# Kernel tuning notes

Hardware: AMD Instinct MI355X
Metric: run time of the kernel (lower is better)

The kernel has to match this reference:

```python
import jax, jax.numpy as jnp
import numpy as np

C = 256
G = 16
KS = 3
K = KS * KS
Cg = C // G
OFFSET_SCALE = 1.0
MLP_HIDDEN = int(C * 4.0)
EPS = 1e-5


def layer_norm(x, w, b):
    mu = jnp.mean(x, axis=-1, keepdims=True)
    xc = x - mu
    var = jnp.mean(xc * xc, axis=-1, keepdims=True)
    return xc * jax.lax.rsqrt(var + EPS) * w + b


def setup_inputs() -> dict:
    key = jax.random.key(0)
    ks = jax.random.split(key, 16)
    B, H, W = 4, 64, 64
    s = 0.02
    inp = {
        "x": jax.random.normal(ks[0], (B, C, H, W), dtype=jnp.float32),
        "norm1_w": jnp.ones((C,), jnp.float32),
        "norm1_b": jnp.zeros((C,), jnp.float32),
        "vproj_w": s * jax.random.normal(ks[1], (C, C), jnp.float32),
        "vproj_b": jnp.zeros((C,), jnp.float32),
        "om_w": s * jax.random.normal(ks[2], (G * 3 * K, C), jnp.float32),
        "om_b": jnp.zeros((G * 3 * K,), jnp.float32),
        "oproj_w": s * jax.random.normal(ks[3], (C, C), jnp.float32),
        "oproj_b": jnp.zeros((C,), jnp.float32),
        "norm2_w": jnp.ones((C,), jnp.float32),
        "norm2_b": jnp.zeros((C,), jnp.float32),
        "fc1_w": s * jax.random.normal(ks[4], (MLP_HIDDEN, C), jnp.float32),
        "fc1_b": jnp.zeros((MLP_HIDDEN,), jnp.float32),
        "fc2_w": s * jax.random.normal(ks[5], (C, MLP_HIDDEN), jnp.float32),
        "fc2_b": jnp.zeros((C,), jnp.float32),
    }
    return inp


def dcnv4(xn, H, W, vproj_w, vproj_b, om_w, om_b, oproj_w, oproj_b):
    # xn: (B, L, C) layer-normed input, L = H*W row-major (h, w)
    B, L, _ = xn.shape
    v = (xn @ vproj_w.T + vproj_b).reshape(B, L, G, Cg)          # value, grouped
    om = (xn @ om_w.T + om_b).reshape(B, L, G, 3 * K)
    off = om[..., : 2 * K].reshape(B, L, G, K, 2)                # (x, y) offsets
    mask = om[..., 2 * K :]                                      # (B, L, G, K) - DCNv4: no softmax

    # kernel grid (dilation 1, 3x3 centered)
    d = jnp.arange(KS, dtype=jnp.float32) - (KS - 1) / 2.0
    dy, dx = jnp.meshgrid(d, d, indexing="ij")                  # (KS, KS)
    dx = dx.reshape(K)
    dy = dy.reshape(K)

    base_x = jnp.tile(jnp.arange(W, dtype=jnp.float32), H)       # (L,)
    base_y = jnp.repeat(jnp.arange(H, dtype=jnp.float32), W)     # (L,)

    # absolute sampling coords in pixel units, (B, L, G, K)
    px = base_x[None, :, None, None] + OFFSET_SCALE * (dx[None, None, None, :] + off[..., 0])
    py = base_y[None, :, None, None] + OFFSET_SCALE * (dy[None, None, None, :] + off[..., 1])

    x0 = jnp.floor(px)
    y0 = jnp.floor(py)
    tx = px - x0
    ty = py - y0
    x0i = x0.astype(jnp.int32)
    y0i = y0.astype(jnp.int32)

    bi = jnp.arange(B)[:, None, None, None]
    gi = jnp.arange(G)[None, None, :, None]

    def gather(xi, yi):
        valid = (xi >= 0) & (xi < W) & (yi >= 0) & (yi < H)
        lin = jnp.clip(yi, 0, H - 1) * W + jnp.clip(xi, 0, W - 1)
        g = v[bi, lin, gi]                                       # (B, L, G, K, Cg)
        return g * valid[..., None].astype(v.dtype)

    samp = (
        gather(x0i, y0i) * ((1 - tx) * (1 - ty))[..., None]
        + gather(x0i + 1, y0i) * (tx * (1 - ty))[..., None]
        + gather(x0i, y0i + 1) * ((1 - tx) * ty)[..., None]
        + gather(x0i + 1, y0i + 1) * (tx * ty)[..., None]
    )
    out = jnp.einsum("blgkc,blgk->blgc", samp, mask).reshape(B, L, C)
    return out @ oproj_w.T + oproj_b


def reference(x, norm1_w, norm1_b, vproj_w, vproj_b, om_w, om_b, oproj_w, oproj_b,
              norm2_w, norm2_b, fc1_w, fc1_b, fc2_w, fc2_b):
    B, _, H, W = x.shape
    shortcut = x.transpose(0, 2, 3, 1).reshape(B, H * W, C)
    xn = layer_norm(shortcut, norm1_w, norm1_b)
    x1 = shortcut + dcnv4(xn, H, W, vproj_w, vproj_b, om_w, om_b, oproj_w, oproj_b)
    h = layer_norm(x1, norm2_w, norm2_b)
    h = jax.nn.gelu(h @ fc1_w.T + fc1_b, approximate=False) @ fc2_w.T + fc2_b
    x2 = x1 + h
    return x2.reshape(B, H, W, C).transpose(0, 3, 1, 2)
```

## Files before the change

### kernel.cpp

```cpp
#include <hip/hip_runtime.h>
#include <math.h>

#define Cc    256
#define Gg    16
#define KK    9
#define Cgc   16
#define Hh    64
#define Ww    64
#define Ll    4096
#define Bb    4
#define HID   1024
#define OMN   432
#define NTOK  16384

typedef unsigned short ushort_t;
typedef __attribute__((ext_vector_type(8))) short bf16x8;
typedef __attribute__((ext_vector_type(4))) float f32x4;

__device__ __forceinline__ ushort_t f2bf(float x) {
    unsigned int u = __float_as_uint(x);
    unsigned int r = (u + 0x7fffu + ((u >> 16) & 1u)) >> 16;
    return (ushort_t)r;
}
__device__ __forceinline__ float bf2f(ushort_t h) {
    return __uint_as_float(((unsigned int)h) << 16);
}
__device__ __forceinline__ void split2(float x, ushort_t& h, ushort_t& l) {
    h = f2bf(x);
    l = f2bf(x - bf2f(h));
}

__global__ void transpose_k(const float* __restrict__ in, float* __restrict__ out,
                            int Rows, int Cols) {
    __shared__ float tile[32][33];
    int b  = blockIdx.z;
    int c0 = blockIdx.x * 32;
    int r0 = blockIdx.y * 32;
    int tx = threadIdx.x;
    int ty = threadIdx.y;
    const float* ip = in + ((size_t)b * Rows + r0) * Cols + c0;
#pragma unroll
    for (int i = 0; i < 32; i += 8)
        tile[ty + i][tx] = ip[(size_t)(ty + i) * Cols + tx];
    __syncthreads();
    float* op = out + ((size_t)b * Cols + c0) * Rows + r0;
#pragma unroll
    for (int i = 0; i < 32; i += 8)
        op[(size_t)(ty + i) * Rows + tx] = tile[tx][ty + i];
}

__global__ void layernorm_k(const float* __restrict__ in, const float* __restrict__ w,
                            const float* __restrict__ bvec,
                            ushort_t* __restrict__ outh, ushort_t* __restrict__ outl) {
    int row  = blockIdx.x * 4 + (threadIdx.x >> 6);
    int lane = threadIdx.x & 63;
    const float4* ip = (const float4*)(in + (size_t)row * Cc);
    float4 v = ip[lane];
    float s  = v.x + v.y + v.z + v.w;
    float sq = v.x * v.x + v.y * v.y + v.z * v.z + v.w * v.w;
#pragma unroll
    for (int m = 1; m < 64; m <<= 1) {
        s  += __shfl_xor(s, m);
        sq += __shfl_xor(sq, m);
    }
    float mu  = s * (1.0f / Cc);
    float var = sq * (1.0f / Cc) - mu * mu;
    float rs  = rsqrtf(var + 1e-5f);
    float4 wv = ((const float4*)w)[lane];
    float4 bv = ((const float4*)bvec)[lane];
    float o0 = (v.x - mu) * rs * wv.x + bv.x;
    float o1 = (v.y - mu) * rs * wv.y + bv.y;
    float o2 = (v.z - mu) * rs * wv.z + bv.z;
    float o3 = (v.w - mu) * rs * wv.w + bv.w;
    ushort4 hv, lv;
    split2(o0, hv.x, lv.x);
    split2(o1, hv.y, lv.y);
    split2(o2, hv.z, lv.z);
    split2(o3, hv.w, lv.w);
    ((ushort4*)(outh + (size_t)row * Cc))[lane] = hv;
    ((ushort4*)(outl + (size_t)row * Cc))[lane] = lv;
}

__global__ void wsplit_k(const float* __restrict__ in,
                         ushort_t* __restrict__ h, ushort_t* __restrict__ l) {
    int i = blockIdx.x * 256 + threadIdx.x;
    float4 v = ((const float4*)in)[i];
    ushort4 hv, lv;
    split2(v.x, hv.x, lv.x);
    split2(v.y, hv.y, lv.y);
    split2(v.z, hv.z, lv.z);
    split2(v.w, hv.w, lv.w);
    ((ushort4*)h)[i] = hv;
    ((ushort4*)l)[i] = lv;
}

template<bool RES, int ACT, int OUT>
__global__ __launch_bounds__(512)
void gemm_mfma_k(const ushort_t* __restrict__ Ah, const ushort_t* __restrict__ Al,
                 const ushort_t* __restrict__ Wh, const ushort_t* __restrict__ Wl,
                 const float* __restrict__ bias, const float* __restrict__ res,
                 float* __restrict__ Cout, ushort_t* __restrict__ Ch,
                 ushort_t* __restrict__ Cl, int M, int N, int Kd) {
    __shared__ ushort_t AsH[128][40];
    __shared__ ushort_t AsL[128][40];
    __shared__ ushort_t BsH[128][40];
    __shared__ ushort_t BsL[128][40];

    int tid  = threadIdx.x;
    int lane = tid & 63;
    int wave = tid >> 6;
    int wm = wave >> 1;
    int wn = wave & 1;
    int m0 = blockIdx.x * 128;
    int n0 = blockIdx.y * 128;

    f32x4 acc[2][4];
#pragma unroll
    for (int i = 0; i < 2; ++i)
#pragma unroll
        for (int j = 0; j < 4; ++j)
#pragma unroll
            for (int r = 0; r < 4; ++r) acc[i][j][r] = 0.0f;

    int lr = tid >> 2;
    int lc = tid & 3;

    int fr = lane & 15;
    int ko = (lane >> 4) * 8;

    for (int k0 = 0; k0 < Kd; k0 += 32) {
        {
            const ushort_t* p = Ah + (size_t)(m0 + lr) * Kd + k0 + lc * 8;
            const ushort_t* q = Al + (size_t)(m0 + lr) * Kd + k0 + lc * 8;
            *(bf16x8*)&AsH[lr][lc * 8] = *(const bf16x8*)p;
            *(bf16x8*)&AsL[lr][lc * 8] = *(const bf16x8*)q;
        }
        {
            bf16x8 z;
#pragma unroll
            for (int t = 0; t < 8; ++t) z[t] = 0;
            int n1 = n0 + lr;
            bf16x8 bh = z, bl = z;
            if (n1 < N) {
                bh = *(const bf16x8*)(Wh + (size_t)n1 * Kd + k0 + lc * 8);
                bl = *(const bf16x8*)(Wl + (size_t)n1 * Kd + k0 + lc * 8);
            }
            *(bf16x8*)&BsH[lr][lc * 8] = bh;
            *(bf16x8*)&BsL[lr][lc * 8] = bl;
        }
        __syncthreads();

        bf16x8 ah[2], al[2], bh[4], bl[4];
#pragma unroll
        for (int i = 0; i < 2; ++i) {
            ah[i] = *(const bf16x8*)&AsH[wm * 32 + i * 16 + fr][ko];
            al[i] = *(const bf16x8*)&AsL[wm * 32 + i * 16 + fr][ko];
        }
#pragma unroll
        for (int j = 0; j < 4; ++j) {
            bh[j] = *(const bf16x8*)&BsH[wn * 64 + j * 16 + fr][ko];
            bl[j] = *(const bf16x8*)&BsL[wn * 64 + j * 16 + fr][ko];
        }
#pragma unroll
        for (int i = 0; i < 2; ++i)
#pragma unroll
            for (int j = 0; j < 4; ++j) {
                acc[i][j] = __builtin_amdgcn_mfma_f32_16x16x32_bf16(ah[i], bh[j], acc[i][j], 0, 0, 0);
                acc[i][j] = __builtin_amdgcn_mfma_f32_16x16x32_bf16(ah[i], bl[j], acc[i][j], 0, 0, 0);
                acc[i][j] = __builtin_amdgcn_mfma_f32_16x16x32_bf16(al[i], bh[j], acc[i][j], 0, 0, 0);
            }
        __syncthreads();
    }

#pragma unroll
    for (int j = 0; j < 4; ++j) {
        int n = n0 + wn * 64 + j * 16 + fr;
        if (n >= N) continue;
        float bv = bias[n];
#pragma unroll
        for (int i = 0; i < 2; ++i) {
            int rb = m0 + wm * 32 + i * 16 + ((lane >> 4) << 2);
            float vr[4];
#pragma unroll
            for (int r = 0; r < 4; ++r) {
                float v = acc[i][j][r] + bv;
                if (ACT == 1) v = 0.5f * v * (1.0f + erff(v * 0.70710678118654752f));
                if (RES) v += res[(size_t)(rb + r) * N + n];
                vr[r] = v;
            }
            if (OUT == 0) {
#pragma unroll
                for (int r = 0; r < 4; ++r)
                    Cout[(size_t)(rb + r) * N + n] = vr[r];
            } else if (OUT == 1) {
#pragma unroll
                for (int r = 0; r < 4; ++r) {
                    ushort_t h, l;
                    split2(vr[r], h, l);
                    Ch[(size_t)(rb + r) * N + n] = h;
                    Cl[(size_t)(rb + r) * N + n] = l;
                }
            } else {
                int b = rb >> 12;
                int l = rb & 4095;
                float4 o = make_float4(vr[0], vr[1], vr[2], vr[3]);
                *(float4*)&Cout[((size_t)b * Cc + n) * Ll + l] = o;
            }
        }
    }
}

__global__ __launch_bounds__(256)
void dcn_sample_k(const float* __restrict__ v, const float* __restrict__ om,
                  ushort_t* __restrict__ outh, ushort_t* __restrict__ outl) {
    int token = blockIdx.x;
    int b = token >> 12;
    int l = token & 4095;
    int h = l >> 6, w = l & 63;
    int g  = threadIdx.x >> 4;
    int cg = threadIdx.x & 15;

    const float* omp = om + (size_t)token * OMN + g * 27;
    const float* vb  = v + (size_t)b * Ll * Cc + g * Cgc + cg;

    float acc = 0.0f;
#pragma unroll
    for (int k = 0; k < 9; ++k) {
        float dx = (float)(k % 3) - 1.0f;
        float dy = (float)(k / 3) - 1.0f;
        float px = (float)w + dx + omp[2 * k];
        float py = (float)h + dy + omp[2 * k + 1];
        float mk = omp[18 + k];
        float x0f = floorf(px), y0f = floorf(py);
        float tx = px - x0f, ty = py - y0f;
        int x0 = (int)x0f, y0 = (int)y0f;

        float tap[4];
#pragma unroll
        for (int t = 0; t < 4; ++t) {
            int xi = x0 + (t & 1);
            int yi = y0 + (t >> 1);
            bool valid = (xi >= 0) && (xi < Ww) && (yi >= 0) && (yi < Hh);
            int xc = min(max(xi, 0), Ww - 1);
            int yc = min(max(yi, 0), Hh - 1);
            float val = vb[(size_t)(yc * Ww + xc) * Cc];
            tap[t] = valid ? val : 0.0f;
        }
        float s = tap[0] * (1.0f - tx) * (1.0f - ty)
                + tap[1] * tx * (1.0f - ty)
                + tap[2] * (1.0f - tx) * ty
                + tap[3] * tx * ty;
        acc = fmaf(mk, s, acc);
    }
    size_t idx = (size_t)token * Cc + g * Cgc + cg;
    ushort_t hh, ll;
    split2(acc, hh, ll);
    outh[idx] = hh;
    outl[idx] = ll;
}

extern "C" void kernel_launch(void* const* d_in, const int* in_sizes, int n_in,
                              void* d_out, int out_size, void* d_ws, size_t ws_size,
                              hipStream_t stream) {
    const float* x        = (const float*)d_in[0];
    const float* n1w      = (const float*)d_in[1];
    const float* n1b      = (const float*)d_in[2];
    const float* vproj_w  = (const float*)d_in[3];
    const float* vproj_b  = (const float*)d_in[4];
    const float* om_w     = (const float*)d_in[5];
    const float* om_b     = (const float*)d_in[6];
    const float* oproj_w  = (const float*)d_in[7];
    const float* oproj_b  = (const float*)d_in[8];
    const float* n2w      = (const float*)d_in[9];
    const float* n2b      = (const float*)d_in[10];
    const float* fc1_w    = (const float*)d_in[11];
    const float* fc1_b    = (const float*)d_in[12];
    const float* fc2_w    = (const float*)d_in[13];
    const float* fc2_b    = (const float*)d_in[14];
    float* out = (float*)d_out;

    char* base = (char*)d_ws;
    float*    s0   = (float*)base;
    char* pB = base + (size_t)16777216;
    ushort_t* xnh  = (ushort_t*)pB;
    ushort_t* xnl  = xnh + (size_t)NTOK * Cc;
    char* pC = pB + (size_t)16777216;
    float*    vbuf = (float*)pC;
    char* pD = pC + (size_t)16777216;
    float*    om   = (float*)pD;
    ushort_t* xn2h = (ushort_t*)pD;
    ushort_t* xn2l = xn2h + (size_t)NTOK * Cc;
    char* pE = pD + (size_t)28311552;
    float*    x1   = (float*)pE;
    char* pF = pE + (size_t)16777216;
    ushort_t* hh   = (ushort_t*)pF;
    ushort_t* hl   = hh + (size_t)NTOK * HID;
    char* pG = pF + (size_t)67108864;
    ushort_t* wp   = (ushort_t*)pG;
    ushort_t* vpWh = wp;              ushort_t* vpWl = vpWh + 65536;
    ushort_t* omWh = vpWl + 65536;    ushort_t* omWl = omWh + 110592;
    ushort_t* opWh = omWl + 110592;   ushort_t* opWl = opWh + 65536;
    ushort_t* f1Wh = opWl + 65536;    ushort_t* f1Wl = f1Wh + 262144;
    ushort_t* f2Wh = f1Wl + 262144;   ushort_t* f2Wl = f2Wh + 262144;

    dim3 tblk(32, 8);

    wsplit_k<<<64,  256, 0, stream>>>(vproj_w, vpWh, vpWl);
    wsplit_k<<<108, 256, 0, stream>>>(om_w,    omWh, omWl);
    wsplit_k<<<64,  256, 0, stream>>>(oproj_w, opWh, opWl);
    wsplit_k<<<256, 256, 0, stream>>>(fc1_w,   f1Wh, f1Wl);
    wsplit_k<<<256, 256, 0, stream>>>(fc2_w,   f2Wh, f2Wl);

    transpose_k<<<dim3(Ll / 32, Cc / 32, Bb), tblk, 0, stream>>>(x, s0, Cc, Ll);

    layernorm_k<<<NTOK / 4, 256, 0, stream>>>(s0, n1w, n1b, xnh, xnl);

    gemm_mfma_k<false, 0, 0><<<dim3(NTOK / 128, 2), 512, 0, stream>>>(
        xnh, xnl, vpWh, vpWl, vproj_b, nullptr, vbuf, nullptr, nullptr, NTOK, Cc, Cc);

    gemm_mfma_k<false, 0, 0><<<dim3(NTOK / 128, 4), 512, 0, stream>>>(
        xnh, xnl, omWh, omWl, om_b, nullptr, om, nullptr, nullptr, NTOK, OMN, Cc);

    dcn_sample_k<<<NTOK, 256, 0, stream>>>(vbuf, om, xnh, xnl);

    gemm_mfma_k<true, 0, 0><<<dim3(NTOK / 128, 2), 512, 0, stream>>>(
        xnh, xnl, opWh, opWl, oproj_b, s0, x1, nullptr, nullptr, NTOK, Cc, Cc);

    layernorm_k<<<NTOK / 4, 256, 0, stream>>>(x1, n2w, n2b, xn2h, xn2l);

    gemm_mfma_k<false, 1, 1><<<dim3(NTOK / 128, 8), 512, 0, stream>>>(
        xn2h, xn2l, f1Wh, f1Wl, fc1_b, nullptr, nullptr, hh, hl, NTOK, HID, Cc);

    gemm_mfma_k<true, 0, 2><<<dim3(NTOK / 128, 2), 512, 0, stream>>>(
        hh, hl, f2Wh, f2Wl, fc2_b, x1, out, nullptr, nullptr, NTOK, Cc, HID);
}
```

Baseline: 342.0 us.

## Double-buffer GEMM via direct global-to-LDS loads, merge vproj/om GEMMs and weight splits

The GEMM kernel is rewritten to load tiles straight from global memory into LDS with global_load_lds, using a swizzled layout and double buffering so the next K tile loads while MFMAs run on the current one. The value and offset/mask projections are merged into one GEMM over a concatenated weight matrix (N=688) with split outputs. The five weight-split launches become one kernel, and the DCN sampler stages each token's offset/mask row in shared memory. Together these aim to cut per-iteration load stalls, launch count, and redundant reads of the input activations, at the cost of a more complex addressing scheme and some padded work in the merged GEMM.

```diff
diff --git a/kernel.cpp b/kernel.cpp
--- a/kernel.cpp
+++ b/kernel.cpp
@@ -28,6 +28,12 @@
 __device__ __forceinline__ void split2(float x, ushort_t& h, ushort_t& l) {
     h = f2bf(x);
     l = f2bf(x - bf2f(h));
+}
+
+__device__ __forceinline__ void gl_lds16(const ushort_t* g, ushort_t* l) {
+    __builtin_amdgcn_global_load_lds(
+        (__attribute__((address_space(1))) void*)g,
+        (__attribute__((address_space(3))) void*)l, 16, 0, 0);
 }
 
 __global__ void transpose_k(const float* __restrict__ in, float* __restrict__ out,
@@ -81,38 +87,61 @@
     ((ushort4*)(outl + (size_t)row * Cc))[lane] = lv;
 }
 
-__global__ void wsplit_k(const float* __restrict__ in,
-                         ushort_t* __restrict__ h, ushort_t* __restrict__ l) {
-    int i = blockIdx.x * 256 + threadIdx.x;
-    float4 v = ((const float4*)in)[i];
+__global__ void wsplit_all_k(const float* __restrict__ w0, const float* __restrict__ w1,
+                             const float* __restrict__ w2, const float* __restrict__ w3,
+                             const float* __restrict__ w4,
+                             ushort_t* __restrict__ d0h, ushort_t* __restrict__ d0l,
+                             ushort_t* __restrict__ d2h, ushort_t* __restrict__ d2l,
+                             ushort_t* __restrict__ d3h, ushort_t* __restrict__ d3l,
+                             ushort_t* __restrict__ d4h, ushort_t* __restrict__ d4l) {
+    int blk = blockIdx.x;
+    const float* src; ushort_t* dh; ushort_t* dl; int off;
+    if (blk < 64)       { src = w0; dh = d0h;          dl = d0l;          off = blk; }
+    else if (blk < 172) { src = w1; dh = d0h + 65536;  dl = d0l + 65536;  off = blk - 64; }
+    else if (blk < 236) { src = w2; dh = d2h;          dl = d2l;          off = blk - 172; }
+    else if (blk < 492) { src = w3; dh = d3h;          dl = d3l;          off = blk - 236; }
+    else                { src = w4; dh = d4h;          dl = d4l;          off = blk - 492; }
+    int i = off * 256 + threadIdx.x;
+    float4 v = ((const float4*)src)[i];
     ushort4 hv, lv;
     split2(v.x, hv.x, lv.x);
     split2(v.y, hv.y, lv.y);
     split2(v.z, hv.z, lv.z);
     split2(v.w, hv.w, lv.w);
-    ((ushort4*)h)[i] = hv;
-    ((ushort4*)l)[i] = lv;
+    ((ushort4*)dh)[i] = hv;
+    ((ushort4*)dl)[i] = lv;
 }
 
 template<bool RES, int ACT, int OUT>
 __global__ __launch_bounds__(512)
-void gemm_mfma_k(const ushort_t* __restrict__ Ah, const ushort_t* __restrict__ Al,
-                 const ushort_t* __restrict__ Wh, const ushort_t* __restrict__ Wl,
-                 const float* __restrict__ bias, const float* __restrict__ res,
-                 float* __restrict__ Cout, ushort_t* __restrict__ Ch,
-                 ushort_t* __restrict__ Cl, int M, int N, int Kd) {
-    __shared__ ushort_t AsH[128][40];
-    __shared__ ushort_t AsL[128][40];
-    __shared__ ushort_t BsH[128][40];
-    __shared__ ushort_t BsL[128][40];
+void gemm2_k(const ushort_t* __restrict__ Ah, const ushort_t* __restrict__ Al,
+             const ushort_t* __restrict__ Wh, const ushort_t* __restrict__ Wl,
+             const float* __restrict__ bias, const float* __restrict__ bias2,
+             const float* __restrict__ res,
+             float* __restrict__ Cout, float* __restrict__ Cout2,
+             ushort_t* __restrict__ Ch, ushort_t* __restrict__ Cl,
+             int M, int N, int Kd) {
+    __shared__ ushort_t sA[2][2][128 * 32];
+    __shared__ ushort_t sB[2][2][128 * 32];
 
     int tid  = threadIdx.x;
-    int lane = tid & 63;
-    int wave = tid >> 6;
-    int wm = wave >> 1;
-    int wn = wave & 1;
-    int m0 = blockIdx.x * 128;
-    int n0 = blockIdx.y * 128;
+    int l    = tid & 63;
+    int w    = tid >> 6;
+    int wm   = w >> 1;
+    int wn   = w & 1;
+    int m0   = blockIdx.x * 128;
+    int n0   = blockIdx.y * 128;
+
+    int sr = (w << 4) + (l >> 2);
+    int sc = (l & 3) ^ (sr & 3);
+    size_t aoff = (size_t)(m0 + sr) * Kd + sc * 8;
+    int brow = n0 + sr; if (brow > N - 1) brow = N - 1;
+    size_t boff = (size_t)brow * Kd + sc * 8;
+    int lbase = w << 9;
+
+    int fr  = l & 15;
+    int kc  = l >> 4;
+    int sl8 = ((kc ^ (fr & 3)) << 3);
 
     f32x4 acc[2][4];
 #pragma unroll
@@ -122,64 +151,59 @@
 #pragma unroll
             for (int r = 0; r < 4; ++r) acc[i][j][r] = 0.0f;
 
-    int lr = tid >> 2;
-    int lc = tid & 3;
-
-    int fr = lane & 15;
-    int ko = (lane >> 4) * 8;
-
-    for (int k0 = 0; k0 < Kd; k0 += 32) {
-        {
-            const ushort_t* p = Ah + (size_t)(m0 + lr) * Kd + k0 + lc * 8;
-            const ushort_t* q = Al + (size_t)(m0 + lr) * Kd + k0 + lc * 8;
-            *(bf16x8*)&AsH[lr][lc * 8] = *(const bf16x8*)p;
-            *(bf16x8*)&AsL[lr][lc * 8] = *(const bf16x8*)q;
-        }
-        {
-            bf16x8 z;
-#pragma unroll
-            for (int t = 0; t < 8; ++t) z[t] = 0;
-            int n1 = n0 + lr;
-            bf16x8 bh = z, bl = z;
-            if (n1 < N) {
-                bh = *(const bf16x8*)(Wh + (size_t)n1 * Kd + k0 + lc * 8);
-                bl = *(const bf16x8*)(Wl + (size_t)n1 * Kd + k0 + lc * 8);
-            }
-            *(bf16x8*)&BsH[lr][lc * 8] = bh;
-            *(bf16x8*)&BsL[lr][lc * 8] = bl;
-        }
-        __syncthreads();
-
-        bf16x8 ah[2], al[2], bh[4], bl[4];
+    int nt = Kd >> 5;
+
+    gl_lds16(Ah + aoff, &sA[0][0][lbase]);
+    gl_lds16(Al + aoff, &sA[0][1][lbase]);
+    gl_lds16(Wh + boff, &sB[0][0][lbase]);
+    gl_lds16(Wl + boff, &sB[0][1][lbase]);
+    __syncthreads();
+
+    int cur = 0;
+    for (int t = 0; t < nt; ++t) {
+        if (t + 1 < nt) {
+            size_t ko = (size_t)(t + 1) << 5;
+            int nb = cur ^ 1;
+            gl_lds16(Ah + aoff + ko, &sA[nb][0][lbase]);
+            gl_lds16(Al + aoff + ko, &sA[nb][1][lbase]);
+            gl_lds16(Wh + boff + ko, &sB[nb][0][lbase]);
+            gl_lds16(Wl + boff + ko, &sB[nb][1][lbase]);
+        }
+        bf16x8 a_h[2], a_l[2], b_h[4], b_l[4];
 #pragma unroll
         for (int i = 0; i < 2; ++i) {
-            ah[i] = *(const bf16x8*)&AsH[wm * 32 + i * 16 + fr][ko];
-            al[i] = *(const bf16x8*)&AsL[wm * 32 + i * 16 + fr][ko];
+            int R = wm * 32 + i * 16 + fr;
+            a_h[i] = *(const bf16x8*)&sA[cur][0][R * 32 + sl8];
+            a_l[i] = *(const bf16x8*)&sA[cur][1][R * 32 + sl8];
         }
 #pragma unroll
         for (int j = 0; j < 4; ++j) {
-            bh[j] = *(const bf16x8*)&BsH[wn * 64 + j * 16 + fr][ko];
-            bl[j] = *(const bf16x8*)&BsL[wn * 64 + j * 16 + fr][ko];
+            int R = wn * 64 + j * 16 + fr;
+            b_h[j] = *(const bf16x8*)&sB[cur][0][R * 32 + sl8];
+            b_l[j] = *(const bf16x8*)&sB[cur][1][R * 32 + sl8];
         }
 #pragma unroll
         for (int i = 0; i < 2; ++i)
 #pragma unroll
             for (int j = 0; j < 4; ++j) {
-                acc[i][j] = __builtin_amdgcn_mfma_f32_16x16x32_bf16(ah[i], bh[j], acc[i][j], 0, 0, 0);
-                acc[i][j] = __builtin_amdgcn_mfma_f32_16x16x32_bf16(ah[i], bl[j], acc[i][j], 0, 0, 0);
-                acc[i][j] = __builtin_amdgcn_mfma_f32_16x16x32_bf16(al[i], bh[j], acc[i][j], 0, 0, 0);
+                acc[i][j] = __builtin_amdgcn_mfma_f32_16x16x32_bf16(a_h[i], b_h[j], acc[i][j], 0, 0, 0);
+                acc[i][j] = __builtin_amdgcn_mfma_f32_16x16x32_bf16(a_h[i], b_l[j], acc[i][j], 0, 0, 0);
+                acc[i][j] = __builtin_amdgcn_mfma_f32_16x16x32_bf16(a_l[i], b_h[j], acc[i][j], 0, 0, 0);
             }
         __syncthreads();
+        cur ^= 1;
     }
 
 #pragma unroll
     for (int j = 0; j < 4; ++j) {
         int n = n0 + wn * 64 + j * 16 + fr;
         if (n >= N) continue;
-        float bv = bias[n];
+        float bv;
+        if (OUT == 3) bv = (n < 256) ? bias[n] : bias2[n - 256];
+        else          bv = bias[n];
 #pragma unroll
         for (int i = 0; i < 2; ++i) {
-            int rb = m0 + wm * 32 + i * 16 + ((lane >> 4) << 2);
+            int rb = m0 + wm * 32 + i * 16 + ((l >> 4) << 2);
             float vr[4];
 #pragma unroll
             for (int r = 0; r < 4; ++r) {
@@ -195,16 +219,26 @@
             } else if (OUT == 1) {
 #pragma unroll
                 for (int r = 0; r < 4; ++r) {
-                    ushort_t h, l;
-                    split2(vr[r], h, l);
+                    ushort_t h, lo;
+                    split2(vr[r], h, lo);
                     Ch[(size_t)(rb + r) * N + n] = h;
-                    Cl[(size_t)(rb + r) * N + n] = l;
+                    Cl[(size_t)(rb + r) * N + n] = lo;
                 }
+            } else if (OUT == 2) {
+                int b  = rb >> 12;
+                int li = rb & 4095;
+                float4 o = make_float4(vr[0], vr[1], vr[2], vr[3]);
+                *(float4*)&Cout[((size_t)b * Cc + n) * Ll + li] = o;
             } else {
-                int b = rb >> 12;
-                int l = rb & 4095;
-                float4 o = make_float4(vr[0], vr[1], vr[2], vr[3]);
-                *(float4*)&Cout[((size_t)b * Cc + n) * Ll + l] = o;
+                if (n < 256) {
+#pragma unroll
+                    for (int r = 0; r < 4; ++r)
+                        Cout[(size_t)(rb + r) * 256 + n] = vr[r];
+                } else {
+#pragma unroll
+                    for (int r = 0; r < 4; ++r)
+                        Cout2[(size_t)(rb + r) * OMN + (n - 256)] = vr[r];
+                }
             }
         }
     }
@@ -213,14 +247,20 @@
 __global__ __launch_bounds__(256)
 void dcn_sample_k(const float* __restrict__ v, const float* __restrict__ om,
                   ushort_t* __restrict__ outh, ushort_t* __restrict__ outl) {
+    __shared__ float omL[OMN];
     int token = blockIdx.x;
+    int tid = threadIdx.x;
+    if (tid < OMN - 256) omL[256 + tid] = om[(size_t)token * OMN + 256 + tid];
+    omL[tid] = om[(size_t)token * OMN + tid];
+    __syncthreads();
+
     int b = token >> 12;
-    int l = token & 4095;
-    int h = l >> 6, w = l & 63;
-    int g  = threadIdx.x >> 4;
-    int cg = threadIdx.x & 15;
-
-    const float* omp = om + (size_t)token * OMN + g * 27;
+    int lidx = token & 4095;
+    int h = lidx >> 6, w = lidx & 63;
+    int g  = tid >> 4;
+    int cg = tid & 15;
+
+    const float* omp = omL + g * 27;
     const float* vb  = v + (size_t)b * Ll * Cc + g * Cgc + cg;
 
     float acc = 0.0f;
@@ -297,40 +337,38 @@
     ushort_t* hl   = hh + (size_t)NTOK * HID;
     char* pG = pF + (size_t)67108864;
     ushort_t* wp   = (ushort_t*)pG;
-    ushort_t* vpWh = wp;              ushort_t* vpWl = vpWh + 65536;
-    ushort_t* omWh = vpWl + 65536;    ushort_t* omWl = omWh + 110592;
-    ushort_t* opWh = omWl + 110592;   ushort_t* opWl = opWh + 65536;
+    ushort_t* mWh  = wp;
+    ushort_t* mWl  = mWh + 176128;
+    ushort_t* opWh = mWl + 176128;    ushort_t* opWl = opWh + 65536;
     ushort_t* f1Wh = opWl + 65536;    ushort_t* f1Wl = f1Wh + 262144;
     ushort_t* f2Wh = f1Wl + 262144;   ushort_t* f2Wl = f2Wh + 262144;
 
     dim3 tblk(32, 8);
 
-    wsplit_k<<<64,  256, 0, stream>>>(vproj_w, vpWh, vpWl);
-    wsplit_k<<<108, 256, 0, stream>>>(om_w,    omWh, omWl);
-    wsplit_k<<<64,  256, 0, stream>>>(oproj_w, opWh, opWl);
-    wsplit_k<<<256, 256, 0, stream>>>(fc1_w,   f1Wh, f1Wl);
-    wsplit_k<<<256, 256, 0, stream>>>(fc2_w,   f2Wh, f2Wl);
+    wsplit_all_k<<<748, 256, 0, stream>>>(vproj_w, om_w, oproj_w, fc1_w, fc2_w,
+                                          mWh, mWl, opWh, opWl, f1Wh, f1Wl, f2Wh, f2Wl);
 
     transpose_k<<<dim3(Ll / 32, Cc / 32, Bb), tblk, 0, stream>>>(x, s0, Cc, Ll);
 
     layernorm_k<<<NTOK / 4, 256, 0, stream>>>(s0, n1w, n1b, xnh, xnl);
 
-    gemm_mfma_k<false, 0, 0><<<dim3(NTOK / 128, 2), 512, 0, stream>>>(
-        xnh, xnl, vpWh, vpWl, vproj_b, nullptr, vbuf, nullptr, nullptr, NTOK, Cc, Cc);
-
-    gemm_mfma_k<false, 0, 0><<<dim3(NTOK / 128, 4), 512, 0, stream>>>(
-        xnh, xnl, omWh, omWl, om_b, nullptr, om, nullptr, nullptr, NTOK, OMN, Cc);
+    gemm2_k<false, 0, 3><<<dim3(NTOK / 128, 6), 512, 0, stream>>>(
+        xnh, xnl, mWh, mWl, vproj_b, om_b, nullptr,
+        vbuf, om, nullptr, nullptr, NTOK, 688, Cc);
 
     dcn_sample_k<<<NTOK, 256, 0, stream>>>(vbuf, om, xnh, xnl);
 
-    gemm_mfma_k<true, 0, 0><<<dim3(NTOK / 128, 2), 512, 0, stream>>>(
-        xnh, xnl, opWh, opWl, oproj_b, s0, x1, nullptr, nullptr, NTOK, Cc, Cc);
+    gemm2_k<true, 0, 0><<<dim3(NTOK / 128, 2), 512, 0, stream>>>(
+        xnh, xnl, opWh, opWl, oproj_b, nullptr, s0,
+        x1, nullptr, nullptr, nullptr, NTOK, Cc, Cc);
 
     layernorm_k<<<NTOK / 4, 256, 0, stream>>>(x1, n2w, n2b, xn2h, xn2l);
 
-    gemm_mfma_k<false, 1, 1><<<dim3(NTOK / 128, 8), 512, 0, stream>>>(
-        xn2h, xn2l, f1Wh, f1Wl, fc1_b, nullptr, nullptr, hh, hl, NTOK, HID, Cc);
-
-    gemm_mfma_k<true, 0, 2><<<dim3(NTOK / 128, 2), 512, 0, stream>>>(
-        hh, hl, f2Wh, f2Wl, fc2_b, x1, out, nullptr, nullptr, NTOK, Cc, HID);
-}
+    gemm2_k<false, 1, 1><<<dim3(NTOK / 128, 8), 512, 0, stream>>>(
+        xn2h, xn2l, f1Wh, f1Wl, fc1_b, nullptr, nullptr,
+        nullptr, nullptr, hh, hl, NTOK, HID, Cc);
+
+    gemm2_k<true, 0, 2><<<dim3(NTOK / 128, 2), 512, 0, stream>>>(
+        hh, hl, f2Wh, f2Wl, fc2_b, nullptr, x1,
+        out, nullptr, nullptr, nullptr, NTOK, Cc, HID);
+}
```

New measurement: 316.5 us. 1.08x faster.
